# Kernel optimization log

Measured on AMD Instinct MI355X. Metric: run time of the kernel, lower is better.

Reference implementation:

```python
import jax, jax.numpy as jnp
import numpy as np

B, N, D = 32768, 20, 13  # batch, n_humans, rotated-state dim (last input channel is mask)
LAYERS = {
    'm1': [(D, 150), (150, 100)],          # mlp1, last_relu=True
    'm2': [(100, 100), (100, 50)],          # mlp2
    'at': [(200, 100), (100, 100), (100, 1)],  # attention (global state concat -> 2*100 in)
    'hp': [(100, 100), (100, 100), (100, 7)],  # human_state_predictor (50*2 in)
}

def _mlp(x, params, last_relu=False):
    n = len(params)
    for i, (W, b) in enumerate(params):
        x = x @ W + b
        if i < n - 1 or last_relu:
            x = jax.nn.relu(x)
    return x

def setup_inputs() -> dict:
    key = jax.random.key(0)
    ks, kx, km = jax.random.split(key, 3)
    inp = {}
    for name, shapes in LAYERS.items():
        for i, (fi, fo) in enumerate(shapes):
            kw, kb, ks = jax.random.split(jax.random.fold_in(ks, i), 3)
            inp[f'{name}_w{i}'] = jax.random.normal(kw, (fi, fo), jnp.float32) / jnp.sqrt(float(fi))
            inp[f'{name}_b{i}'] = jnp.zeros((fo,), jnp.float32)
    x = jax.random.normal(kx, (B, N, D + 1), jnp.float32)
    mask = (jax.random.uniform(km, (B, N)) < 0.9).astype(jnp.float32)  # 0/1 visibility mask
    inp['state'] = x.at[..., -1].set(mask)
    return inp

def reference(state, m1_w0, m1_b0, m1_w1, m1_b1,
              m2_w0, m2_b0, m2_w1, m2_b1,
              at_w0, at_b0, at_w1, at_b1, at_w2, at_b2,
              hp_w0, hp_b0, hp_w1, hp_b1, hp_w2, hp_b2):
    x, mask = state[..., :-1], state[..., -1]        # (B,N,D), (B,N)
    h1 = _mlp(x, [(m1_w0, m1_b0), (m1_w1, m1_b1)], last_relu=True)   # (B,N,100)
    h2 = _mlp(h1, [(m2_w0, m2_b0), (m2_w1, m2_b1)])                   # (B,N,50)

    # masked mean-pool global state (NaN-on-empty zeroed, as in torch)
    msum = jnp.sum(mask, axis=1, keepdims=True)                       # (B,1)
    mw = jnp.where(msum > 0, mask / jnp.where(msum > 0, msum, 1.0), 0.0)
    global_state = jnp.sum(mw[..., None] * h1, axis=1, keepdims=True) # (B,1,100)
    att_in = jnp.concatenate([h1, jnp.broadcast_to(global_state, h1.shape)], axis=-1)

    scores = _mlp(att_in, [(at_w0, at_b0), (at_w1, at_b1), (at_w2, at_b2)])[..., 0]  # (B,N)
    scores = scores * mask
    se = jnp.exp(scores) * (scores != 0).astype(scores.dtype)
    ssum = jnp.sum(se, axis=1, keepdims=True)
    w = jnp.where(ssum > 0, se / jnp.where(ssum > 0, ssum, 1.0), 0.0)[..., None]  # (B,N,1)

    wsum = jnp.sum(w * h2, axis=1, keepdims=True)                     # (B,1,50)
    joint = jnp.concatenate([h2, jnp.broadcast_to(wsum, h2.shape)], axis=-1)  # (B,N,100)
    return _mlp(joint, [(hp_w0, hp_b0), (hp_w1, hp_b1), (hp_w2, hp_b2)])      # (B,N,7)
```

## Files before the change

kernel.cpp:

```cpp
#include <hip/hip_runtime.h>
#include <hip/hip_bf16.h>


typedef short sx8 __attribute__((ext_vector_type(8)));
typedef short sx4 __attribute__((ext_vector_type(4)));
typedef float fx4 __attribute__((ext_vector_type(4)));
typedef unsigned ux2 __attribute__((ext_vector_type(2)));

#define TB   512
#define NW   8
#define NB   4
#define MTOK 80
#define MT   5
#define CHH  640
#define CHG  128

#define OFF_BUFT 0
#define OFF_BUFA 25600
#define OFF_BUFH 46080
#define OFF_BUFG 56320
#define OFF_BIAS 60416
#define OFF_GRC  63808
#define OFF_WRC  65600
#define OFF_SC   67392
#define OFF_MASK 67712
#define OFF_MSUM 68032
#define OFF_WTM  68048
#define SMEM_BYTES 71120

#define B_M1B0 0
#define B_M1B1 152
#define B_M2B0 256
#define B_M2B1 360
#define B_ATB0 416
#define B_ATB1 520
#define B_HPB0 624
#define B_HPB1 728
#define B_HPB2 832

#define WS_M1W0  0
#define WS_M1W1  5120
#define WS_M2W0  23040
#define WS_M2W1  37376
#define WS_ATW0  45568
#define WS_ATW1  59904
#define WS_HPW0  74240
#define WS_HPW1  81408
#define WS_HPW2  95744
#define WS_ATW0H 97792
#define WS_HPW0H 112128
#define WS_ATW2  119296

__device__ __forceinline__ short f2b(float f) {
    unsigned u = __builtin_bit_cast(unsigned, f);
    u += 0x7FFFu + ((u >> 16) & 1u);
    return (short)(u >> 16);
}
__device__ __forceinline__ float b2f(short h) {
    unsigned u = ((unsigned)(unsigned short)h) << 16;
    return __builtin_bit_cast(float, u);
}
__device__ __forceinline__ sx4 pack4(fx4 v) {
    __hip_bfloat162 lo = __float22bfloat162_rn(make_float2(v[0], v[1]));
    __hip_bfloat162 hi = __float22bfloat162_rn(make_float2(v[2], v[3]));
    ux2 p;
    unsigned ulo, uhi;
    __builtin_memcpy(&ulo, &lo, 4);
    __builtin_memcpy(&uhi, &hi, 4);
    p[0] = ulo; p[1] = uhi;
    return __builtin_bit_cast(sx4, p);
}

__device__ __forceinline__ void stg(const float* __restrict__ W, int N,
                                    int KR, int KPAD, int NR, int Nsrc,
                                    short* dst, int gtid, int gsz) {
    int K8 = KPAD >> 3;
    for (int idx = gtid; idx < NR * K8; idx += gsz) {
        int k8 = idx / NR, nl = idx - k8 * NR;
        int k0 = k8 << 3;
        sx8 h;
        #pragma unroll
        for (int i = 0; i < 8; ++i) {
            int k = k0 + i;
            float v = (k < KR && nl < Nsrc) ? W[k * N + nl] : 0.f;
            h[i] = f2b(v);
        }
        *(sx8*)(dst + (k8 * NR + nl) * 8) = h;
    }
}

__global__ void stage_weights(
    const float* __restrict__ m1w0, const float* __restrict__ m1w1,
    const float* __restrict__ m2w0, const float* __restrict__ m2w1,
    const float* __restrict__ atw0, const float* __restrict__ atw1,
    const float* __restrict__ hpw0, const float* __restrict__ hpw1,
    const float* __restrict__ hpw2, const float* __restrict__ atw2,
    short* __restrict__ ws)
{
    int gtid = blockIdx.x * blockDim.x + threadIdx.x;
    int gsz = gridDim.x * blockDim.x;
    stg(m1w0, 150, 13, 32, 160, 150, ws + WS_M1W0, gtid, gsz);
    stg(m1w1, 100, 150, 160, 112, 100, ws + WS_M1W1, gtid, gsz);
    stg(m2w0, 100, 100, 128, 112, 100, ws + WS_M2W0, gtid, gsz);
    stg(m2w1, 50, 100, 128, 64, 50, ws + WS_M2W1, gtid, gsz);
    stg(atw0, 100, 100, 128, 112, 100, ws + WS_ATW0, gtid, gsz);
    stg(atw1, 100, 100, 128, 112, 100, ws + WS_ATW1, gtid, gsz);
    stg(hpw0, 100, 50, 64, 112, 100, ws + WS_HPW0, gtid, gsz);
    stg(hpw1, 100, 100, 128, 112, 100, ws + WS_HPW1, gtid, gsz);
    stg(hpw2, 7, 100, 128, 16, 7, ws + WS_HPW2, gtid, gsz);
    stg(atw0 + 100 * 100, 100, 100, 128, 112, 100, ws + WS_ATW0H, gtid, gsz);
    stg(hpw0 + 50 * 100, 100, 50, 64, 112, 100, ws + WS_HPW0H, gtid, gsz);
    stg(atw2, 1, 100, 128, 16, 1, ws + WS_ATW2, gtid, gsz);
}

template <int KT, int NT, bool RELU, bool UINIT>
__device__ __forceinline__ void gemm(const short* __restrict__ wg, int NR,
                                     const short* bIn, short* bOut,
                                     const float* initp, int initBstride,
                                     int wave, int lm, int lq) {
    constexpr int NG = (NT + 1) / 2;
    constexpr int NU = NG * 2;
    for (int u = wave; u < NU; u += NW) {
        int ng = u >> 1, mh = u & 1;
        int nt0 = ng * 2, nt1 = nt0 + 1;
        bool hasN1 = !((NT & 1) && (ng == NG - 1));
        sx8 a0[KT], a1[KT];
        #pragma unroll
        for (int kt = 0; kt < KT; ++kt)
            a0[kt] = *(const sx8*)(wg + ((kt * 4 + lq) * NR + nt0 * 16 + lm) * 8);
        if (hasN1) {
            #pragma unroll
            for (int kt = 0; kt < KT; ++kt)
                a1[kt] = *(const sx8*)(wg + ((kt * 4 + lq) * NR + nt1 * 16 + lm) * 8);
        }
        int n0l0 = nt0 * 16 + lq * 4;
        int n0l1 = nt1 * 16 + lq * 4;
        fx4 ib0, ib1;
        if (UINIT) {
            ib0 = *(const fx4*)(initp + n0l0);
            if (hasN1) ib1 = *(const fx4*)(initp + n0l1);
        }
        int mstart = mh ? 3 : 0;
        int mcount = mh ? 2 : 3;
        #pragma unroll 3
        for (int mi = 0; mi < mcount; ++mi) {
            int mt = mstart + mi;
            int tok = mt * 16 + lm;
            sx8 bfr[KT];
            #pragma unroll
            for (int kt = 0; kt < KT; ++kt)
                bfr[kt] = *(const sx8*)(bIn + (kt * 4 + lq) * CHH + tok * 8);
            fx4 acc0, acc1;
            if (UINIT) acc0 = ib0;
            else acc0 = *(const fx4*)(initp + (tok / 20) * initBstride + n0l0);
            if (hasN1) {
                if (UINIT) acc1 = ib1;
                else acc1 = *(const fx4*)(initp + (tok / 20) * initBstride + n0l1);
            }
            #pragma unroll
            for (int kt = 0; kt < KT; ++kt) {
                acc0 = __builtin_amdgcn_mfma_f32_16x16x32_bf16(a0[kt], bfr[kt], acc0, 0, 0, 0);
                if (hasN1)
                    acc1 = __builtin_amdgcn_mfma_f32_16x16x32_bf16(a1[kt], bfr[kt], acc1, 0, 0, 0);
            }
            if (RELU) {
                #pragma unroll
                for (int r = 0; r < 4; ++r) acc0[r] = fmaxf(acc0[r], 0.f);
            }
            *(sx4*)(bOut + (nt0 * 2 + (lq >> 1)) * CHH + tok * 8 + (lq & 1) * 4) = pack4(acc0);
            if (hasN1) {
                if (RELU) {
                    #pragma unroll
                    for (int r = 0; r < 4; ++r) acc1[r] = fmaxf(acc1[r], 0.f);
                }
                *(sx4*)(bOut + (nt1 * 2 + (lq >> 1)) * CHH + tok * 8 + (lq & 1) * 4) = pack4(acc1);
            }
        }
    }
}

template <int KT, int NT>
__device__ __forceinline__ void gemmR(const short* __restrict__ wg, int NR,
                                      const short* bG, float* outF,
                                      const float* biasp,
                                      int wave, int lm, int lq) {
    constexpr int NG = (NT + 1) / 2;
    for (int u = wave; u < NG; u += NW) {
        int nt0 = u * 2, nt1 = nt0 + 1;
        bool hasN1 = !((NT & 1) && (u == NG - 1));
        sx8 a0[KT], a1[KT], bfr[KT];
        #pragma unroll
        for (int kt = 0; kt < KT; ++kt) {
            a0[kt] = *(const sx8*)(wg + ((kt * 4 + lq) * NR + nt0 * 16 + lm) * 8);
            bfr[kt] = *(const sx8*)(bG + (kt * 4 + lq) * CHG + lm * 8);
        }
        if (hasN1) {
            #pragma unroll
            for (int kt = 0; kt < KT; ++kt)
                a1[kt] = *(const sx8*)(wg + ((kt * 4 + lq) * NR + nt1 * 16 + lm) * 8);
        }
        int n0l0 = nt0 * 16 + lq * 4;
        int n0l1 = nt1 * 16 + lq * 4;
        fx4 acc0 = *(const fx4*)(biasp + n0l0);
        fx4 acc1;
        if (hasN1) acc1 = *(const fx4*)(biasp + n0l1);
        #pragma unroll
        for (int kt = 0; kt < KT; ++kt) {
            acc0 = __builtin_amdgcn_mfma_f32_16x16x32_bf16(a0[kt], bfr[kt], acc0, 0, 0, 0);
            if (hasN1)
                acc1 = __builtin_amdgcn_mfma_f32_16x16x32_bf16(a1[kt], bfr[kt], acc1, 0, 0, 0);
        }
        if (lm < NB) {
            *(fx4*)(outF + lm * 112 + n0l0) = acc0;
            if (hasN1) *(fx4*)(outF + lm * 112 + n0l1) = acc1;
        }
    }
}

template <int NT>
__device__ __forceinline__ void gemmT(const short* __restrict__ act,
                                      const short* __restrict__ wT,
                                      short* __restrict__ bG,
                                      int wave, int lm, int lq) {
    for (int nt = wave; nt < NT; nt += NW) {
        int j = nt * 16 + lm;
        const short* ap = act + (j >> 3) * CHH + (j & 7);
        fx4 acc = {0.f, 0.f, 0.f, 0.f};
        #pragma unroll
        for (int kt = 0; kt < 3; ++kt) {
            int tok0 = kt * 32 + lq * 8;
            int tok0e = (tok0 < MTOK) ? tok0 : 0;
            sx8 a;
            #pragma unroll
            for (int i = 0; i < 8; ++i) {
                int ii = (i + lq * 2) & 7;
                a[i] = ap[(tok0e + ii) * 8];
            }
            sx8 b = *(const sx8*)(wT + lm * 96 + tok0);
            acc = __builtin_amdgcn_mfma_f32_16x16x32_bf16(a, b, acc, 0, 0, 0);
        }
        if (lm < NB) {
            *(sx4*)(bG + (nt * 2 + (lq >> 1)) * CHG + lm * 8 + (lq & 1) * 4) = pack4(acc);
        }
    }
}

__device__ __forceinline__ void zpad(short* buf, int tid) {
    for (int i = tid; i < 160; i += TB) {
        sx8 z = {0, 0, 0, 0, 0, 0, 0, 0};
        *(sx8*)(buf + 14 * CHH + i * 8) = z;
    }
}

__global__ __launch_bounds__(TB, 4) void sp_mfma_bf16(
    const float* __restrict__ state,
    const float* __restrict__ m1b0, const float* __restrict__ m1b1,
    const float* __restrict__ m2b0, const float* __restrict__ m2b1,
    const float* __restrict__ atb0, const float* __restrict__ atb1,
    const float* __restrict__ atb2,
    const float* __restrict__ hpb0, const float* __restrict__ hpb1,
    const float* __restrict__ hpb2,
    const short* __restrict__ ws,
    float* __restrict__ out)
{
    __shared__ __align__(16) unsigned char smem[SMEM_BYTES];
    short* bufT  = (short*)(smem + OFF_BUFT);
    short* bufA  = (short*)(smem + OFF_BUFA);
    short* bufH2 = (short*)(smem + OFF_BUFH);
    short* bufG  = (short*)(smem + OFF_BUFG);
    float* biasv = (float*)(smem + OFF_BIAS);
    float* grc   = (float*)(smem + OFF_GRC);
    float* wrc   = (float*)(smem + OFF_WRC);
    float* scv   = (float*)(smem + OFF_SC);
    float* maskv = (float*)(smem + OFF_MASK);
    float* msum  = (float*)(smem + OFF_MSUM);
    short* wTm   = (short*)(smem + OFF_WTM);

    const int tid  = threadIdx.x;
    const int lane = tid & 63;
    const int wave = tid >> 6;
    const int lm   = lane & 15;
    const int lq   = lane >> 4;
    const long gt0 = (long)blockIdx.x * MTOK;

    {
        const float* bs[9] = {m1b0, m1b1, m2b0, m2b1, atb0, atb1, hpb0, hpb1, hpb2};
        const int off[9] = {B_M1B0, B_M1B1, B_M2B0, B_M2B1, B_ATB0, B_ATB1, B_HPB0, B_HPB1, B_HPB2};
        const int sz[9]  = {150, 100, 100, 50, 100, 100, 100, 100, 7};
        const int pd[9]  = {152, 104, 104, 56, 104, 104, 104, 104, 16};
        #pragma unroll
        for (int r = 0; r < 9; ++r)
            for (int i = tid; i < pd[r]; i += TB)
                biasv[off[r] + i] = (i < sz[r]) ? bs[r][i] : 0.f;
        if (tid < MTOK) maskv[tid] = state[(gt0 + tid) * 14 + 13];
        for (int t = tid; t < 256; t += TB) {
            sx8 z = {0, 0, 0, 0, 0, 0, 0, 0};
            *(sx8*)(bufG + t * 8) = z;
        }
        for (int idx = tid; idx < MTOK * 4; idx += TB) {
            int row = idx >> 2, seg = idx & 3;
            const float* xp = state + (gt0 + row) * 14;
            sx8 h;
            #pragma unroll
            for (int i = 0; i < 8; ++i) {
                int k = seg * 8 + i;
                float v = (k < 13) ? xp[k] : 0.f;
                h[i] = f2b(v);
            }
            *(sx8*)(bufA + seg * CHH + row * 8) = h;
        }
    }
    __syncthreads();

    if (tid < NB) {
        float s = 0.f;
        #pragma unroll
        for (int n = 0; n < 20; ++n) s += maskv[tid * 20 + n];
        msum[tid] = s;
    }
    gemm<1, 10, true, true>(ws + WS_M1W0, 160, bufA, bufT, biasv + B_M1B0, 0,
                            wave, lm, lq);
    __syncthreads();

    gemm<5, 7, true, true>(ws + WS_M1W1, 112, bufT, bufA, biasv + B_M1B1, 0,
                           wave, lm, lq);
    zpad(bufA, tid);
    for (int t = tid; t < 1536; t += TB) {
        int b = t / 96, tp = t - b * 96;
        int tau = (tp & ~7) | ((tp + ((tp >> 3) & 3) * 2) & 7);
        float v = 0.f;
        if (b < NB && tau < MTOK && tau / 20 == b) {
            float ms = msum[b];
            v = (ms > 0.f) ? maskv[tau] / ms : 0.f;
        }
        wTm[t] = f2b(v);
    }
    __syncthreads();

    gemmT<7>(bufA, wTm, bufG, wave, lm, lq);
    gemm<4, 7, true, true>(ws + WS_M2W0, 112, bufA, bufT, biasv + B_M2B0, 0,
                           wave, lm, lq);
    zpad(bufT, tid);
    __syncthreads();

    gemmR<4, 7>(ws + WS_ATW0H, 112, bufG, grc, biasv + B_ATB0, wave, lm, lq);
    gemm<4, 4, false, true>(ws + WS_M2W1, 64, bufT, bufH2, biasv + B_M2B1, 0,
                            (wave + 4) & 7, lm, lq);
    __syncthreads();

    gemm<4, 7, true, false>(ws + WS_ATW0, 112, bufA, bufT, grc, 112,
                            wave, lm, lq);
    __syncthreads();

    gemm<4, 7, true, true>(ws + WS_ATW1, 112, bufT, bufA, biasv + B_ATB1, 0,
                           wave, lm, lq);
    __syncthreads();

    {
        float atb2s = atb2[0];
        sx8 afr[4];
        #pragma unroll
        for (int kt = 0; kt < 4; ++kt)
            afr[kt] = *(const sx8*)(ws + WS_ATW2 + ((kt * 4 + lq) * 16 + lm) * 8);
        for (int mt = wave; mt < MT; mt += NW) {
            int tok = mt * 16 + lm;
            fx4 acc = {0.f, 0.f, 0.f, 0.f};
            const short* bp = bufA + tok * 8;
            #pragma unroll
            for (int kt = 0; kt < 4; ++kt) {
                sx8 b = *(const sx8*)(bp + (kt * 4 + lq) * CHH);
                acc = __builtin_amdgcn_mfma_f32_16x16x32_bf16(afr[kt], b, acc, 0, 0, 0);
            }
            if (lq == 0) {
                float s = (acc[0] + atb2s) * maskv[tok];
                scv[tok] = (s != 0.f) ? __expf(s) : 0.f;
            }
        }
    }
    __syncthreads();

    for (int t = tid; t < 1536; t += TB) {
        int b = t / 96, tp = t - b * 96;
        int tau = (tp & ~7) | ((tp + ((tp >> 3) & 3) * 2) & 7);
        float v = 0.f;
        if (b < NB && tau < MTOK && tau / 20 == b) {
            float ss = 0.f;
            #pragma unroll
            for (int n = 0; n < 20; ++n) ss += scv[b * 20 + n];
            v = (ss > 0.f) ? scv[tau] / ss : 0.f;
        }
        wTm[t] = f2b(v);
    }
    __syncthreads();

    gemmT<4>(bufH2, wTm, bufG, wave, lm, lq);
    __syncthreads();

    gemmR<2, 7>(ws + WS_HPW0H, 112, bufG, wrc, biasv + B_HPB0, wave, lm, lq);
    __syncthreads();

    gemm<2, 7, true, false>(ws + WS_HPW0, 112, bufH2, bufT, wrc, 112,
                            wave, lm, lq);
    __syncthreads();

    gemm<4, 7, true, true>(ws + WS_HPW1, 112, bufT, bufA, biasv + B_HPB1, 0,
                           wave, lm, lq);
    __syncthreads();

    {
        sx8 afr[4];
        #pragma unroll
        for (int kt = 0; kt < 4; ++kt)
            afr[kt] = *(const sx8*)(ws + WS_HPW2 + ((kt * 4 + lq) * 16 + lm) * 8);
        fx4 ib = *(const fx4*)(biasv + B_HPB2 + lq * 4);
        for (int mt = wave; mt < MT; mt += NW) {
            int tok = mt * 16 + lm;
            fx4 acc = ib;
            const short* bp = bufA + tok * 8;
            #pragma unroll
            for (int kt = 0; kt < 4; ++kt) {
                sx8 b = *(const sx8*)(bp + (kt * 4 + lq) * CHH);
                acc = __builtin_amdgcn_mfma_f32_16x16x32_bf16(afr[kt], b, acc, 0, 0, 0);
            }
            #pragma unroll
            for (int r = 0; r < 4; ++r) {
                int n = lq * 4 + r;
                if (n < 7) out[(gt0 + tok) * 7 + n] = acc[r];
            }
        }
    }
}

extern "C" void kernel_launch(void* const* d_in, const int* in_sizes, int n_in,
                              void* d_out, int out_size, void* d_ws, size_t ws_size,
                              hipStream_t stream) {
    int si = 20, wb = 0;
    if (in_sizes[0] > 1000000) { si = 0; wb = 1; }
    const float* state = (const float*)d_in[si];
    const float* W[20];
    for (int i = 0; i < 20; ++i) W[i] = (const float*)d_in[wb + i];
    float* out = (float*)d_out;
    short* ws = (short*)d_ws;
    int Btot = in_sizes[si] / (20 * 14);
    int nblocks = Btot / NB;

    hipLaunchKernelGGL(stage_weights, dim3(128), dim3(256), 0, stream,
        W[0], W[2], W[4], W[6], W[8], W[10], W[14], W[16], W[18], W[12], ws);

    hipLaunchKernelGGL(sp_mfma_bf16, dim3(nblocks), dim3(TB), 0, stream,
        state,
        W[1], W[3],
        W[5], W[7],
        W[9], W[11],
        W[13],
        W[15], W[17], W[19],
        ws, out);
}
```

Before: 412.4 us.

## Replace pooling GEMMs with per-wave scalar reductions and fuse softmax pooling

The masked mean-pool and the attention-weighted pool were each done by building a transposed weight matrix in shared memory and running a small MFMA GEMM. Both are replaced with direct per-wave dot products over the 20 humans. The attention-score layer, scalar softmax and weighted sum are fused into one block that uses wave shuffles. This removes several __syncthreads barriers and the wTm/scv staging buffers, and cuts shared memory use. The cost is scalar FMA work on bf16-converted values instead of MFMA, and an fp32 copy of the attention output weight loaded into LDS.

```diff
diff --git a/kernel.cpp b/kernel.cpp
--- a/kernel.cpp
+++ b/kernel.cpp
@@ -22,11 +22,10 @@
 #define OFF_BIAS 60416
 #define OFF_GRC  63808
 #define OFF_WRC  65600
-#define OFF_SC   67392
-#define OFF_MASK 67712
-#define OFF_MSUM 68032
-#define OFF_WTM  68048
-#define SMEM_BYTES 71120
+#define OFF_MASK 67392
+#define OFF_MSUM 67712
+#define OFF_ATW2F 67728
+#define SMEM_BYTES 68176
 
 #define B_M1B0 0
 #define B_M1B1 152
@@ -217,34 +216,6 @@
     }
 }
 
-template <int NT>
-__device__ __forceinline__ void gemmT(const short* __restrict__ act,
-                                      const short* __restrict__ wT,
-                                      short* __restrict__ bG,
-                                      int wave, int lm, int lq) {
-    for (int nt = wave; nt < NT; nt += NW) {
-        int j = nt * 16 + lm;
-        const short* ap = act + (j >> 3) * CHH + (j & 7);
-        fx4 acc = {0.f, 0.f, 0.f, 0.f};
-        #pragma unroll
-        for (int kt = 0; kt < 3; ++kt) {
-            int tok0 = kt * 32 + lq * 8;
-            int tok0e = (tok0 < MTOK) ? tok0 : 0;
-            sx8 a;
-            #pragma unroll
-            for (int i = 0; i < 8; ++i) {
-                int ii = (i + lq * 2) & 7;
-                a[i] = ap[(tok0e + ii) * 8];
-            }
-            sx8 b = *(const sx8*)(wT + lm * 96 + tok0);
-            acc = __builtin_amdgcn_mfma_f32_16x16x32_bf16(a, b, acc, 0, 0, 0);
-        }
-        if (lm < NB) {
-            *(sx4*)(bG + (nt * 2 + (lq >> 1)) * CHG + lm * 8 + (lq & 1) * 4) = pack4(acc);
-        }
-    }
-}
-
 __device__ __forceinline__ void zpad(short* buf, int tid) {
     for (int i = tid; i < 160; i += TB) {
         sx8 z = {0, 0, 0, 0, 0, 0, 0, 0};
@@ -257,7 +228,7 @@
     const float* __restrict__ m1b0, const float* __restrict__ m1b1,
     const float* __restrict__ m2b0, const float* __restrict__ m2b1,
     const float* __restrict__ atb0, const float* __restrict__ atb1,
-    const float* __restrict__ atb2,
+    const float* __restrict__ atb2, const float* __restrict__ atw2,
     const float* __restrict__ hpb0, const float* __restrict__ hpb1,
     const float* __restrict__ hpb2,
     const short* __restrict__ ws,
@@ -271,10 +242,9 @@
     float* biasv = (float*)(smem + OFF_BIAS);
     float* grc   = (float*)(smem + OFF_GRC);
     float* wrc   = (float*)(smem + OFF_WRC);
-    float* scv   = (float*)(smem + OFF_SC);
     float* maskv = (float*)(smem + OFF_MASK);
     float* msum  = (float*)(smem + OFF_MSUM);
-    short* wTm   = (short*)(smem + OFF_WTM);
+    float* atw2f = (float*)(smem + OFF_ATW2F);
 
     const int tid  = threadIdx.x;
     const int lane = tid & 63;
@@ -292,6 +262,8 @@
         for (int r = 0; r < 9; ++r)
             for (int i = tid; i < pd[r]; i += TB)
                 biasv[off[r] + i] = (i < sz[r]) ? bs[r][i] : 0.f;
+        for (int i = tid; i < 104; i += TB)
+            atw2f[i] = (i < 100) ? atw2[i] : 0.f;
         if (tid < MTOK) maskv[tid] = state[(gt0 + tid) * 14 + 13];
         for (int t = tid; t < 256; t += TB) {
             sx8 z = {0, 0, 0, 0, 0, 0, 0, 0};
@@ -325,19 +297,25 @@
     gemm<5, 7, true, true>(ws + WS_M1W1, 112, bufT, bufA, biasv + B_M1B1, 0,
                            wave, lm, lq);
     zpad(bufA, tid);
-    for (int t = tid; t < 1536; t += TB) {
-        int b = t / 96, tp = t - b * 96;
-        int tau = (tp & ~7) | ((tp + ((tp >> 3) & 3) * 2) & 7);
-        float v = 0.f;
-        if (b < NB && tau < MTOK && tau / 20 == b) {
-            float ms = msum[b];
-            v = (ms > 0.f) ? maskv[tau] / ms : 0.f;
-        }
-        wTm[t] = f2b(v);
-    }
-    __syncthreads();
-
-    gemmT<7>(bufA, wTm, bufG, wave, lm, lq);
+    __syncthreads();
+
+    {
+        int b = wave & 3, half = wave >> 2;
+        int j = half * 64 + lane;
+        if (j < 112) {
+            float g = 0.f;
+            if (j < 100) {
+                float ms = msum[b];
+                float inv = (ms > 0.f) ? 1.f / ms : 0.f;
+                const short* hp = bufA + (j >> 3) * CHH + (j & 7);
+                #pragma unroll
+                for (int t = 0; t < 20; ++t)
+                    g = fmaf(maskv[b * 20 + t], b2f(hp[(b * 20 + t) * 8]), g);
+                g *= inv;
+            }
+            bufG[(j >> 3) * CHG + b * 8 + (j & 7)] = f2b(g);
+        }
+    }
     gemm<4, 7, true, true>(ws + WS_M2W0, 112, bufA, bufT, biasv + B_M2B0, 0,
                            wave, lm, lq);
     zpad(bufT, tid);
@@ -357,43 +335,39 @@
     __syncthreads();
 
     {
+        int b = wave & 3, half = wave >> 2;
+        int tokb = b * 20;
         float atb2s = atb2[0];
-        sx8 afr[4];
-        #pragma unroll
-        for (int kt = 0; kt < 4; ++kt)
-            afr[kt] = *(const sx8*)(ws + WS_ATW2 + ((kt * 4 + lq) * 16 + lm) * 8);
-        for (int mt = wave; mt < MT; mt += NW) {
-            int tok = mt * 16 + lm;
-            fx4 acc = {0.f, 0.f, 0.f, 0.f};
-            const short* bp = bufA + tok * 8;
-            #pragma unroll
-            for (int kt = 0; kt < 4; ++kt) {
-                sx8 b = *(const sx8*)(bp + (kt * 4 + lq) * CHH);
-                acc = __builtin_amdgcn_mfma_f32_16x16x32_bf16(afr[kt], b, acc, 0, 0, 0);
-            }
-            if (lq == 0) {
-                float s = (acc[0] + atb2s) * maskv[tok];
-                scv[tok] = (s != 0.f) ? __expf(s) : 0.f;
-            }
-        }
-    }
-    __syncthreads();
-
-    for (int t = tid; t < 1536; t += TB) {
-        int b = t / 96, tp = t - b * 96;
-        int tau = (tp & ~7) | ((tp + ((tp >> 3) & 3) * 2) & 7);
-        float v = 0.f;
-        if (b < NB && tau < MTOK && tau / 20 == b) {
-            float ss = 0.f;
-            #pragma unroll
-            for (int n = 0; n < 20; ++n) ss += scv[b * 20 + n];
-            v = (ss > 0.f) ? scv[tau] / ss : 0.f;
-        }
-        wTm[t] = f2b(v);
-    }
-    __syncthreads();
-
-    gemmT<4>(bufH2, wTm, bufG, wave, lm, lq);
+        float se = 0.f;
+        if (lane < 20) {
+            float s = atb2s;
+            const short* bp = bufA + (tokb + lane) * 8;
+            #pragma unroll
+            for (int k8 = 0; k8 < 13; ++k8) {
+                sx8 v = *(const sx8*)(bp + k8 * CHH);
+                #pragma unroll
+                for (int i = 0; i < 8; ++i)
+                    s = fmaf(b2f(v[i]), atw2f[k8 * 8 + i], s);
+            }
+            s *= maskv[tokb + lane];
+            se = (s != 0.f) ? __expf(s) : 0.f;
+        }
+        int j = half * 32 + (lane & 31);
+        bool act = (lane < 32);
+        float ss = 0.f, v = 0.f;
+        const short* hp = bufH2 + (j >> 3) * CHH + (j & 7);
+        #pragma unroll
+        for (int t = 0; t < 20; ++t) {
+            float set = __shfl(se, t, 64);
+            ss += set;
+            if (act && j < 50)
+                v = fmaf(set, b2f(hp[(tokb + t) * 8]), v);
+        }
+        if (act) {
+            float inv = (ss > 0.f) ? 1.f / ss : 0.f;
+            bufG[(j >> 3) * CHG + b * 8 + (j & 7)] = f2b((j < 50) ? v * inv : 0.f);
+        }
+    }
     __syncthreads();
 
     gemmR<2, 7>(ws + WS_HPW0H, 112, bufG, wrc, biasv + B_HPB0, wave, lm, lq);
@@ -452,7 +426,7 @@
         W[1], W[3],
         W[5], W[7],
         W[9], W[11],
-        W[13],
+        W[13], W[12],
         W[15], W[17], W[19],
         ws, out);
 }
```

New measurement: 419.5 us. Within noise of the previous version (+1.7%).

## Prefetch next-layer weight fragments into registers across barriers

Applied to the files above, without the earlier changes.

Weight A-fragments for each upcoming GEMM stage are now loaded from global memory into registers one stage early, before the preceding stage's compute and barrier. New gemmP/gemmRP variants take the preloaded fragments instead of loading them themselves. The aim is to hide global-load latency of the weights behind the previous layer's MFMA work. The cost is higher register pressure, which may reduce occupancy or cause spills.

```diff
diff --git a/kernel.cpp b/kernel.cpp
--- a/kernel.cpp
+++ b/kernel.cpp
@@ -113,6 +113,20 @@
     stg(atw2, 1, 100, 128, 16, 1, ws + WS_ATW2, gtid, gsz);
 }
 
+template <int KT>
+__device__ __forceinline__ void loadApair(const short* __restrict__ wg, int NR,
+                                          int nt0, bool hasN1, int lm, int lq,
+                                          sx8* a0, sx8* a1) {
+    #pragma unroll
+    for (int kt = 0; kt < KT; ++kt)
+        a0[kt] = *(const sx8*)(wg + ((kt * 4 + lq) * NR + nt0 * 16 + lm) * 8);
+    if (hasN1) {
+        #pragma unroll
+        for (int kt = 0; kt < KT; ++kt)
+            a1[kt] = *(const sx8*)(wg + ((kt * 4 + lq) * NR + (nt0 + 1) * 16 + lm) * 8);
+    }
+}
+
 template <int KT, int NT, bool RELU, bool UINIT>
 __device__ __forceinline__ void gemm(const short* __restrict__ wg, int NR,
                                      const short* bIn, short* bOut,
@@ -179,41 +193,88 @@
     }
 }
 
-template <int KT, int NT>
-__device__ __forceinline__ void gemmR(const short* __restrict__ wg, int NR,
-                                      const short* bG, float* outF,
-                                      const float* biasp,
-                                      int wave, int lm, int lq) {
+template <int KT, int NT, bool RELU, bool UINIT>
+__device__ __forceinline__ void gemmP(const sx8* a0, const sx8* a1,
+                                      const short* bIn, short* bOut,
+                                      const float* initp, int initBstride,
+                                      int u, int lm, int lq) {
     constexpr int NG = (NT + 1) / 2;
-    for (int u = wave; u < NG; u += NW) {
-        int nt0 = u * 2, nt1 = nt0 + 1;
-        bool hasN1 = !((NT & 1) && (u == NG - 1));
-        sx8 a0[KT], a1[KT], bfr[KT];
-        #pragma unroll
-        for (int kt = 0; kt < KT; ++kt) {
-            a0[kt] = *(const sx8*)(wg + ((kt * 4 + lq) * NR + nt0 * 16 + lm) * 8);
-            bfr[kt] = *(const sx8*)(bG + (kt * 4 + lq) * CHG + lm * 8);
-        }
+    constexpr int NU = NG * 2;
+    if (u >= NU) return;
+    int ng = u >> 1, mh = u & 1;
+    int nt0 = ng * 2, nt1 = nt0 + 1;
+    bool hasN1 = !((NT & 1) && (ng == NG - 1));
+    int n0l0 = nt0 * 16 + lq * 4;
+    int n0l1 = nt1 * 16 + lq * 4;
+    fx4 ib0, ib1;
+    if (UINIT) {
+        ib0 = *(const fx4*)(initp + n0l0);
+        if (hasN1) ib1 = *(const fx4*)(initp + n0l1);
+    }
+    int mstart = mh ? 3 : 0;
+    int mcount = mh ? 2 : 3;
+    #pragma unroll 3
+    for (int mi = 0; mi < mcount; ++mi) {
+        int mt = mstart + mi;
+        int tok = mt * 16 + lm;
+        sx8 bfr[KT];
+        #pragma unroll
+        for (int kt = 0; kt < KT; ++kt)
+            bfr[kt] = *(const sx8*)(bIn + (kt * 4 + lq) * CHH + tok * 8);
+        fx4 acc0, acc1;
+        if (UINIT) acc0 = ib0;
+        else acc0 = *(const fx4*)(initp + (tok / 20) * initBstride + n0l0);
         if (hasN1) {
-            #pragma unroll
-            for (int kt = 0; kt < KT; ++kt)
-                a1[kt] = *(const sx8*)(wg + ((kt * 4 + lq) * NR + nt1 * 16 + lm) * 8);
-        }
-        int n0l0 = nt0 * 16 + lq * 4;
-        int n0l1 = nt1 * 16 + lq * 4;
-        fx4 acc0 = *(const fx4*)(biasp + n0l0);
-        fx4 acc1;
-        if (hasN1) acc1 = *(const fx4*)(biasp + n0l1);
+            if (UINIT) acc1 = ib1;
+            else acc1 = *(const fx4*)(initp + (tok / 20) * initBstride + n0l1);
+        }
         #pragma unroll
         for (int kt = 0; kt < KT; ++kt) {
             acc0 = __builtin_amdgcn_mfma_f32_16x16x32_bf16(a0[kt], bfr[kt], acc0, 0, 0, 0);
             if (hasN1)
                 acc1 = __builtin_amdgcn_mfma_f32_16x16x32_bf16(a1[kt], bfr[kt], acc1, 0, 0, 0);
         }
-        if (lm < NB) {
-            *(fx4*)(outF + lm * 112 + n0l0) = acc0;
-            if (hasN1) *(fx4*)(outF + lm * 112 + n0l1) = acc1;
-        }
+        if (RELU) {
+            #pragma unroll
+            for (int r = 0; r < 4; ++r) acc0[r] = fmaxf(acc0[r], 0.f);
+        }
+        *(sx4*)(bOut + (nt0 * 2 + (lq >> 1)) * CHH + tok * 8 + (lq & 1) * 4) = pack4(acc0);
+        if (hasN1) {
+            if (RELU) {
+                #pragma unroll
+                for (int r = 0; r < 4; ++r) acc1[r] = fmaxf(acc1[r], 0.f);
+            }
+            *(sx4*)(bOut + (nt1 * 2 + (lq >> 1)) * CHH + tok * 8 + (lq & 1) * 4) = pack4(acc1);
+        }
+    }
+}
+
+template <int KT, int NT>
+__device__ __forceinline__ void gemmRP(const sx8* a0, const sx8* a1,
+                                       const short* bG, float* outF,
+                                       const float* biasp, int u, int lm, int lq) {
+    constexpr int NG = (NT + 1) / 2;
+    if (u >= NG) return;
+    int nt0 = u * 2, nt1 = nt0 + 1;
+    bool hasN1 = !((NT & 1) && (u == NG - 1));
+    sx8 bfr[KT];
+    #pragma unroll
+    for (int kt = 0; kt < KT; ++kt)
+        bfr[kt] = *(const sx8*)(bG + (kt * 4 + lq) * CHG + lm * 8);
+    int n0l0 = nt0 * 16 + lq * 4;
+    int n0l1 = nt1 * 16 + lq * 4;
+    fx4 acc0 = *(const fx4*)(biasp + n0l0);
+    fx4 acc1;
+    if (hasN1) acc1 = *(const fx4*)(biasp + n0l1);
+    #pragma unroll
+    for (int kt = 0; kt < KT; ++kt) {
+        acc0 = __builtin_amdgcn_mfma_f32_16x16x32_bf16(a0[kt], bfr[kt], acc0, 0, 0, 0);
+        if (hasN1)
+            acc1 = __builtin_amdgcn_mfma_f32_16x16x32_bf16(a1[kt], bfr[kt], acc1, 0, 0, 0);
+    }
+    if (lm < NB) {
+        *(fx4*)(outF + lm * 112 + n0l0) = acc0;
+        if (hasN1) *(fx4*)(outF + lm * 112 + n0l1) = acc1;
     }
 }
 
@@ -283,6 +344,9 @@
     const int lq   = lane >> 4;
     const long gt0 = (long)blockIdx.x * MTOK;
 
+    const int png   = wave >> 1;
+    const bool ph1  = (png != 3);
+
     {
         const float* bs[9] = {m1b0, m1b1, m2b0, m2b1, atb0, atb1, hpb0, hpb1, hpb2};
         const int off[9] = {B_M1B0, B_M1B1, B_M2B0, B_M2B1, B_ATB0, B_ATB1, B_HPB0, B_HPB1, B_HPB2};
@@ -322,6 +386,8 @@
                             wave, lm, lq);
     __syncthreads();
 
+    sx8 a4_0[4], a4_1[4];
+    loadApair<4>(ws + WS_M2W0, 112, png * 2, ph1, lm, lq, a4_0, a4_1);
     gemm<5, 7, true, true>(ws + WS_M1W1, 112, bufT, bufA, biasv + B_M1B1, 0,
                            wave, lm, lq);
     zpad(bufA, tid);
@@ -337,31 +403,40 @@
     }
     __syncthreads();
 
+    sx8 a5_0[4], a5_1[4];
+    if (wave < 4)
+        loadApair<4>(ws + WS_ATW0H, 112, wave * 2, wave != 3, lm, lq, a5_0, a5_1);
+    else
+        loadApair<4>(ws + WS_M2W1, 64, ((wave - 4) >> 1) * 2, true, lm, lq, a5_0, a5_1);
     gemmT<7>(bufA, wTm, bufG, wave, lm, lq);
-    gemm<4, 7, true, true>(ws + WS_M2W0, 112, bufA, bufT, biasv + B_M2B0, 0,
-                           wave, lm, lq);
+    gemmP<4, 7, true, true>(a4_0, a4_1, bufA, bufT, biasv + B_M2B0, 0,
+                            wave, lm, lq);
     zpad(bufT, tid);
     __syncthreads();
 
-    gemmR<4, 7>(ws + WS_ATW0H, 112, bufG, grc, biasv + B_ATB0, wave, lm, lq);
-    gemm<4, 4, false, true>(ws + WS_M2W1, 64, bufT, bufH2, biasv + B_M2B1, 0,
-                            (wave + 4) & 7, lm, lq);
-    __syncthreads();
-
-    gemm<4, 7, true, false>(ws + WS_ATW0, 112, bufA, bufT, grc, 112,
+    sx8 a6_0[4], a6_1[4];
+    loadApair<4>(ws + WS_ATW0, 112, png * 2, ph1, lm, lq, a6_0, a6_1);
+    gemmRP<4, 7>(a5_0, a5_1, bufG, grc, biasv + B_ATB0, wave, lm, lq);
+    gemmP<4, 4, false, true>(a5_0, a5_1, bufT, bufH2, biasv + B_M2B1, 0,
+                             (wave + 4) & 7, lm, lq);
+    __syncthreads();
+
+    sx8 a7_0[4], a7_1[4];
+    loadApair<4>(ws + WS_ATW1, 112, png * 2, ph1, lm, lq, a7_0, a7_1);
+    gemmP<4, 7, true, false>(a6_0, a6_1, bufA, bufT, grc, 112,
+                             wave, lm, lq);
+    __syncthreads();
+
+    sx8 afr8[4];
+    #pragma unroll
+    for (int kt = 0; kt < 4; ++kt)
+        afr8[kt] = *(const sx8*)(ws + WS_ATW2 + ((kt * 4 + lq) * 16 + lm) * 8);
+    gemmP<4, 7, true, true>(a7_0, a7_1, bufT, bufA, biasv + B_ATB1, 0,
                             wave, lm, lq);
-    __syncthreads();
-
-    gemm<4, 7, true, true>(ws + WS_ATW1, 112, bufT, bufA, biasv + B_ATB1, 0,
-                           wave, lm, lq);
     __syncthreads();
 
     {
         float atb2s = atb2[0];
-        sx8 afr[4];
-        #pragma unroll
-        for (int kt = 0; kt < 4; ++kt)
-            afr[kt] = *(const sx8*)(ws + WS_ATW2 + ((kt * 4 + lq) * 16 + lm) * 8);
         for (int mt = wave; mt < MT; mt += NW) {
             int tok = mt * 16 + lm;
             fx4 acc = {0.f, 0.f, 0.f, 0.f};
@@ -369,7 +444,7 @@
             #pragma unroll
             for (int kt = 0; kt < 4; ++kt) {
                 sx8 b = *(const sx8*)(bp + (kt * 4 + lq) * CHH);
-                acc = __builtin_amdgcn_mfma_f32_16x16x32_bf16(afr[kt], b, acc, 0, 0, 0);
+                acc = __builtin_amdgcn_mfma_f32_16x16x32_bf16(afr8[kt], b, acc, 0, 0, 0);
             }
             if (lq == 0) {
                 float s = (acc[0] + atb2s) * maskv[tok];
@@ -379,6 +454,10 @@
     }
     __syncthreads();
 
+    sx8 a11_0[2], a11_1[2], a12_0[2], a12_1[2];
+    if (wave < 4)
+        loadApair<2>(ws + WS_HPW0H, 112, wave * 2, wave != 3, lm, lq, a11_0, a11_1);
+    loadApair<2>(ws + WS_HPW0, 112, png * 2, ph1, lm, lq, a12_0, a12_1);
     for (int t = tid; t < 1536; t += TB) {
         int b = t / 96, tp = t - b * 96;
         int tau = (tp & ~7) | ((tp + ((tp >> 3) & 3) * 2) & 7);
@@ -396,22 +475,24 @@
     gemmT<4>(bufH2, wTm, bufG, wave, lm, lq);
     __syncthreads();
 
-    gemmR<2, 7>(ws + WS_HPW0H, 112, bufG, wrc, biasv + B_HPB0, wave, lm, lq);
-    __syncthreads();
-
-    gemm<2, 7, true, false>(ws + WS_HPW0, 112, bufH2, bufT, wrc, 112,
+    gemmRP<2, 7>(a11_0, a11_1, bufG, wrc, biasv + B_HPB0, wave, lm, lq);
+    __syncthreads();
+
+    sx8 a13_0[4], a13_1[4];
+    loadApair<4>(ws + WS_HPW1, 112, png * 2, ph1, lm, lq, a13_0, a13_1);
+    gemmP<2, 7, true, false>(a12_0, a12_1, bufH2, bufT, wrc, 112,
+                             wave, lm, lq);
+    __syncthreads();
+
+    sx8 afr14[4];
+    #pragma unroll
+    for (int kt = 0; kt < 4; ++kt)
+        afr14[kt] = *(const sx8*)(ws + WS_HPW2 + ((kt * 4 + lq) * 16 + lm) * 8);
+    gemmP<4, 7, true, true>(a13_0, a13_1, bufT, bufA, biasv + B_HPB1, 0,
                             wave, lm, lq);
     __syncthreads();
 
-    gemm<4, 7, true, true>(ws + WS_HPW1, 112, bufT, bufA, biasv + B_HPB1, 0,
-                           wave, lm, lq);
-    __syncthreads();
-
     {
-        sx8 afr[4];
-        #pragma unroll
-        for (int kt = 0; kt < 4; ++kt)
-            afr[kt] = *(const sx8*)(ws + WS_HPW2 + ((kt * 4 + lq) * 16 + lm) * 8);
         fx4 ib = *(const fx4*)(biasv + B_HPB2 + lq * 4);
         for (int mt = wave; mt < MT; mt += NW) {
             int tok = mt * 16 + lm;
@@ -420,7 +501,7 @@
             #pragma unroll
             for (int kt = 0; kt < 4; ++kt) {
                 sx8 b = *(const sx8*)(bp + (kt * 4 + lq) * CHH);
-                acc = __builtin_amdgcn_mfma_f32_16x16x32_bf16(afr[kt], b, acc, 0, 0, 0);
+                acc = __builtin_amdgcn_mfma_f32_16x16x32_bf16(afr14[kt], b, acc, 0, 0, 0);
             }
             #pragma unroll
             for (int r = 0; r < 4; ++r) {
```

Result: no change. 417.5 us (+1.2%).
